# Kernel optimization log

Hardware: AMD Instinct MI355X
Metric: run time of the kernel (lower is better)

Reference implementation:

```python
import jax, jax.numpy as jnp
import numpy as np

B, SQ, SK, D, H, DH = 4, 1024, 1024, 1024, 16, 64  # transform_units*head_units == 1024


def setup_inputs() -> dict:
    key = jax.random.key(0)
    ks = jax.random.split(key, 8)
    q = jax.random.normal(ks[0], (B, SQ, D), dtype=jnp.float32)
    v = jax.random.normal(ks[1], (B, SK, D), dtype=jnp.float32)
    q_mask = jax.random.randint(ks[2], (B, SQ), 0, 2).astype(bool).at[:, 0].set(True)
    v_mask = jax.random.randint(ks[3], (B, SK), 0, 2).astype(bool).at[:, 0].set(True)
    s = 0.02
    Wq = jax.random.normal(ks[4], (D, H * DH), dtype=jnp.float32) * s
    Wk = jax.random.normal(ks[5], (D, H * DH), dtype=jnp.float32) * s
    Wv = jax.random.normal(ks[6], (D, H * DH), dtype=jnp.float32) * s
    Wo = jax.random.normal(ks[7], (H * DH, D), dtype=jnp.float32) * s
    bq = jnp.zeros((H * DH,), jnp.float32)
    bk = jnp.zeros((H * DH,), jnp.float32)
    bv = jnp.zeros((H * DH,), jnp.float32)
    bo = jnp.zeros((D,), jnp.float32)
    return {"q": q, "v": v, "q_mask": q_mask, "v_mask": v_mask,
            "Wq": Wq, "bq": bq, "Wk": Wk, "bk": bk, "Wv": Wv, "bv": bv,
            "Wo": Wo, "bo": bo}


def reference(q, v, q_mask, v_mask, Wq, bq, Wk, bk, Wv, bv, Wo, bo):
    # k = v in the original module
    k = v
    # QKV projections; split-last-dim + batch-concat trick == reshape to heads
    Q = (q @ Wq + bq).reshape(B, SQ, H, DH)
    Kh = (k @ Wk + bk).reshape(B, SK, H, DH)
    V = (v @ Wv + bv).reshape(B, SK, H, DH)
    # Keras Attention: unscaled dot-product scores
    scores = jnp.einsum('bqhd,bkhd->bhqk', Q, Kh)  # [B,H,SQ,SK]
    scores = jnp.where(v_mask[:, None, None, :], scores, jnp.float32(-1e9))
    attn = jax.nn.softmax(scores, axis=-1)
    ctx = jnp.einsum('bhqk,bkhd->bqhd', attn, V).reshape(B, SQ, H * DH)
    # Keras Attention zeros masked query positions before output dense
    ctx = ctx * q_mask[:, :, None].astype(ctx.dtype)
    return ctx @ Wo + bo
```

## Files before the change

kernel.cpp:

```cpp
#include <hip/hip_runtime.h>
#include <hip/hip_fp16.h>

typedef __attribute__((ext_vector_type(8))) _Float16 f16x8;
typedef __attribute__((ext_vector_type(4))) float f32x4;

__global__ __launch_bounds__(256) void cvt_kernel(const float* __restrict__ in,
                                                  _Float16* __restrict__ out, int n4) {
  int i = blockIdx.x * 256 + threadIdx.x;
  if (i < n4) {
    float4 f = ((const float4*)in)[i];
    union { _Float16 h[4]; uint2 u; } o;
    o.h[0] = (_Float16)f.x; o.h[1] = (_Float16)f.y;
    o.h[2] = (_Float16)f.z; o.h[3] = (_Float16)f.w;
    *(uint2*)&out[4 * i] = o.u;
  }
}

__global__ __launch_bounds__(256) void transpose_cvt_kernel(const float* __restrict__ W,
                                                            _Float16* __restrict__ WT) {
  __shared__ float tile[32][33];
  int bx = blockIdx.x * 32, by = blockIdx.y * 32;
  int tx = threadIdx.x & 31, ty = threadIdx.x >> 5;
  for (int i = 0; i < 4; i++)
    tile[ty + 8 * i][tx] = W[(size_t)(by + ty + 8 * i) * 1024 + bx + tx];
  __syncthreads();
  for (int i = 0; i < 4; i++)
    WT[(size_t)(bx + ty + 8 * i) * 1024 + by + tx] = (_Float16)tile[tx][ty + 8 * i];
}

template <typename OutT>
__device__ __forceinline__ void gemm_body(const _Float16* __restrict__ A,
                                          const _Float16* __restrict__ BT,
                                          const float* __restrict__ bias,
                                          OutT* __restrict__ C,
                                          int m0, int n0, int K, int N) {
  __shared__ _Float16 Alds[128 * 72];
  __shared__ _Float16 Blds[128 * 72];
  int tid = threadIdx.x, lane = tid & 63, w = tid >> 6;
  int c = lane & 15, g = lane >> 4;
  int wm = (w & 1) * 64, wn = (w >> 1) * 64;

  f32x4 acc[4][4];
  for (int i = 0; i < 4; i++)
    for (int j = 0; j < 4; j++)
      acc[i][j] = (f32x4){0.f, 0.f, 0.f, 0.f};

  for (int kt = 0; kt < K; kt += 64) {
    __syncthreads();
    for (int p = 0; p < 4; p++) {
      int linear = p * 256 + tid;
      int row = linear >> 3, seg = (linear & 7) * 8;
      *(uint4*)&Alds[row * 72 + seg] = *(const uint4*)&A[(size_t)(m0 + row) * K + kt + seg];
      *(uint4*)&Blds[row * 72 + seg] = *(const uint4*)&BT[(size_t)(n0 + row) * K + kt + seg];
    }
    __syncthreads();
    for (int ks = 0; ks < 2; ks++) {
      f16x8 af[4], bf[4];
      for (int i = 0; i < 4; i++)
        af[i] = *(const f16x8*)&Alds[(wm + i * 16 + c) * 72 + ks * 32 + g * 8];
      for (int j = 0; j < 4; j++)
        bf[j] = *(const f16x8*)&Blds[(wn + j * 16 + c) * 72 + ks * 32 + g * 8];
      for (int i = 0; i < 4; i++)
        for (int j = 0; j < 4; j++)
          acc[i][j] = __builtin_amdgcn_mfma_f32_16x16x32_f16(af[i], bf[j], acc[i][j], 0, 0, 0);
    }
  }
  for (int j = 0; j < 4; j++) {
    float bv = bias[n0 + wn + j * 16 + c];
    for (int i = 0; i < 4; i++) {
      int r = m0 + wm + i * 16 + g * 4;
      int cc = n0 + wn + j * 16 + c;
      for (int e = 0; e < 4; e++)
        C[(size_t)(r + e) * N + cc] = (OutT)(acc[i][j][e] + bv);
    }
  }
}

__global__ __launch_bounds__(256, 3) void gemm_qkv_kernel(
    const _Float16* __restrict__ q16, const _Float16* __restrict__ v16,
    const _Float16* __restrict__ WqT, const _Float16* __restrict__ WkT,
    const _Float16* __restrict__ WvT,
    const float* __restrict__ bq, const float* __restrict__ bk, const float* __restrict__ bv,
    _Float16* __restrict__ Q16, _Float16* __restrict__ K16, _Float16* __restrict__ V16) {
  int z = blockIdx.z;
  const _Float16* A = (z == 0) ? q16 : v16;
  const _Float16* BT = (z == 0) ? WqT : ((z == 1) ? WkT : WvT);
  const float* bias = (z == 0) ? bq : ((z == 1) ? bk : bv);
  _Float16* C = (z == 0) ? Q16 : ((z == 1) ? K16 : V16);
  gemm_body<_Float16>(A, BT, bias, C, blockIdx.y * 128, blockIdx.x * 128, 1024, 1024);
}

__global__ __launch_bounds__(256, 3) void gemm_out_kernel(
    const _Float16* __restrict__ ctx16, const _Float16* __restrict__ WoT,
    const float* __restrict__ bo, float* __restrict__ out) {
  gemm_body<float>(ctx16, WoT, bo, out, blockIdx.y * 128, blockIdx.x * 128, 1024, 1024);
}

__global__ __launch_bounds__(256, 2) void attn_kernel(
    const _Float16* __restrict__ Q16, const _Float16* __restrict__ K16,
    const _Float16* __restrict__ V16,
    const int* __restrict__ q_mask, const int* __restrict__ v_mask,
    _Float16* __restrict__ ctx16) {
  int qb = blockIdx.x, h = blockIdx.y, b = blockIdx.z;
  int tid = threadIdx.x, lane = tid & 63, w = tid >> 6;
  int c = lane & 15, g = lane >> 4;

  __shared__ _Float16 Qlds[128][72];
  __shared__ _Float16 Klds[64][72];
  __shared__ _Float16 VTlds[64][72];
  __shared__ _Float16 Plds[4][32][72];
  __shared__ float maskadd[64];
  __shared__ float qmaskf[128];

  const _Float16* Qbase = Q16 + ((size_t)(b * 1024 + qb * 128)) * 1024 + h * 64;
  for (int p = 0; p < 4; p++) {
    int linear = p * 256 + tid;
    int row = linear >> 3, seg = (linear & 7) * 8;
    *(uint4*)&Qlds[row][seg] = *(const uint4*)&Qbase[(size_t)row * 1024 + seg];
  }
  if (tid < 128) qmaskf[tid] = q_mask[b * 1024 + qb * 128 + tid] ? 1.0f : 0.0f;
  __syncthreads();

  f16x8 qf[2][2];
  for (int i = 0; i < 2; i++)
    for (int ks = 0; ks < 2; ks++)
      qf[i][ks] = *(const f16x8*)&Qlds[w * 32 + i * 16 + c][ks * 32 + g * 8];

  float m_run[2][4], l_run[2][4];
  f32x4 acc_o[2][4];
  for (int i = 0; i < 2; i++)
    for (int e = 0; e < 4; e++) { m_run[i][e] = -3e38f; l_run[i][e] = 0.f; }
  for (int i = 0; i < 2; i++)
    for (int jd = 0; jd < 4; jd++)
      acc_o[i][jd] = (f32x4){0.f, 0.f, 0.f, 0.f};

  const _Float16* Kbase = K16 + ((size_t)(b * 1024)) * 1024 + h * 64;
  const _Float16* Vbase = V16 + ((size_t)(b * 1024)) * 1024 + h * 64;

  for (int kb = 0; kb < 16; kb++) {
    __syncthreads();
    for (int p = 0; p < 2; p++) {
      int linear = p * 256 + tid;
      int row = linear >> 3, seg = (linear & 7) * 8;
      *(uint4*)&Klds[row][seg] = *(const uint4*)&Kbase[(size_t)(kb * 64 + row) * 1024 + seg];
      union { uint4 u; _Float16 hh[8]; } dv;
      dv.u = *(const uint4*)&Vbase[(size_t)(kb * 64 + row) * 1024 + seg];
      for (int e = 0; e < 8; e++) VTlds[seg + e][row] = dv.hh[e];
    }
    if (tid < 64) maskadd[tid] = v_mask[b * 1024 + kb * 64 + tid] ? 0.0f : -1e30f;
    __syncthreads();

    f16x8 kf[4][2];
    for (int j = 0; j < 4; j++)
      for (int ks = 0; ks < 2; ks++)
        kf[j][ks] = *(const f16x8*)&Klds[j * 16 + c][ks * 32 + g * 8];
    f32x4 s[2][4];
    for (int i = 0; i < 2; i++)
      for (int j = 0; j < 4; j++) {
        s[i][j] = (f32x4){0.f, 0.f, 0.f, 0.f};
        s[i][j] = __builtin_amdgcn_mfma_f32_16x16x32_f16(qf[i][0], kf[j][0], s[i][j], 0, 0, 0);
        s[i][j] = __builtin_amdgcn_mfma_f32_16x16x32_f16(qf[i][1], kf[j][1], s[i][j], 0, 0, 0);
      }

    for (int i = 0; i < 2; i++) {
      float mx[4], nm[4], sc[4], rs[4];
      for (int e = 0; e < 4; e++) {
        for (int j = 0; j < 4; j++) s[i][j][e] += maskadd[j * 16 + c];
        mx[e] = fmaxf(fmaxf(s[i][0][e], s[i][1][e]), fmaxf(s[i][2][e], s[i][3][e]));
      }
      for (int e = 0; e < 4; e++) {
        for (int xm = 1; xm < 16; xm <<= 1) mx[e] = fmaxf(mx[e], __shfl_xor(mx[e], xm));
        nm[e] = fmaxf(m_run[i][e], mx[e]);
        sc[e] = __expf(m_run[i][e] - nm[e]);
        m_run[i][e] = nm[e];
      }
      for (int e = 0; e < 4; e++) {
        rs[e] = 0.f;
        for (int j = 0; j < 4; j++) {
          float pv = __expf(s[i][j][e] - nm[e]);
          s[i][j][e] = pv;
          rs[e] += pv;
        }
        for (int xm = 1; xm < 16; xm <<= 1) rs[e] += __shfl_xor(rs[e], xm);
        l_run[i][e] = l_run[i][e] * sc[e] + rs[e];
        for (int jd = 0; jd < 4; jd++) acc_o[i][jd][e] *= sc[e];
      }
      for (int j = 0; j < 4; j++)
        for (int e = 0; e < 4; e++)
          Plds[w][i * 16 + g * 4 + e][j * 16 + c] = (_Float16)s[i][j][e];
    }
    __syncthreads();

    f16x8 pf[2], vf[4];
    for (int ks = 0; ks < 2; ks++) {
      for (int i = 0; i < 2; i++)
        pf[i] = *(const f16x8*)&Plds[w][i * 16 + c][ks * 32 + g * 8];
      for (int jd = 0; jd < 4; jd++)
        vf[jd] = *(const f16x8*)&VTlds[jd * 16 + c][ks * 32 + g * 8];
      for (int i = 0; i < 2; i++)
        for (int jd = 0; jd < 4; jd++)
          acc_o[i][jd] = __builtin_amdgcn_mfma_f32_16x16x32_f16(pf[i], vf[jd], acc_o[i][jd], 0, 0, 0);
    }
  }

  size_t orow_base = ((size_t)(b * 1024 + qb * 128 + w * 32)) * 1024 + h * 64;
  for (int i = 0; i < 2; i++) {
    float rsc[4];
    for (int e = 0; e < 4; e++)
      rsc[e] = qmaskf[w * 32 + i * 16 + g * 4 + e] / l_run[i][e];
    for (int jd = 0; jd < 4; jd++)
      for (int e = 0; e < 4; e++) {
        float val = acc_o[i][jd][e] * rsc[e];
        ctx16[orow_base + (size_t)(i * 16 + g * 4 + e) * 1024 + jd * 16 + c] = (_Float16)val;
      }
  }
}

extern "C" void kernel_launch(void* const* d_in, const int* in_sizes, int n_in,
                              void* d_out, int out_size, void* d_ws, size_t ws_size,
                              hipStream_t stream) {
  const float* q  = (const float*)d_in[0];
  const float* v  = (const float*)d_in[1];
  const int* q_mask = (const int*)d_in[2];
  const int* v_mask = (const int*)d_in[3];
  const float* Wq = (const float*)d_in[4];
  const float* bq = (const float*)d_in[5];
  const float* Wk = (const float*)d_in[6];
  const float* bk = (const float*)d_in[7];
  const float* Wv = (const float*)d_in[8];
  const float* bv = (const float*)d_in[9];
  const float* Wo = (const float*)d_in[10];
  const float* bo = (const float*)d_in[11];
  float* out = (float*)d_out;

  _Float16* ws = (_Float16*)d_ws;
  const size_t NE = (size_t)4 * 1024 * 1024;
  _Float16* q16   = ws;
  _Float16* v16   = ws + NE;
  _Float16* Q16   = ws + 2 * NE;
  _Float16* K16   = ws + 3 * NE;
  _Float16* V16   = ws + 4 * NE;
  _Float16* ctx16 = ws + 5 * NE;
  _Float16* WqT   = ws + 6 * NE;
  _Float16* WkT   = WqT + 1024 * 1024;
  _Float16* WvT   = WkT + 1024 * 1024;
  _Float16* WoT   = WvT + 1024 * 1024;

  cvt_kernel<<<4096, 256, 0, stream>>>(q, q16, (int)(NE / 4));
  cvt_kernel<<<4096, 256, 0, stream>>>(v, v16, (int)(NE / 4));
  dim3 tg(32, 32);
  transpose_cvt_kernel<<<tg, 256, 0, stream>>>(Wq, WqT);
  transpose_cvt_kernel<<<tg, 256, 0, stream>>>(Wk, WkT);
  transpose_cvt_kernel<<<tg, 256, 0, stream>>>(Wv, WvT);
  transpose_cvt_kernel<<<tg, 256, 0, stream>>>(Wo, WoT);
  gemm_qkv_kernel<<<dim3(8, 32, 3), 256, 0, stream>>>(q16, v16, WqT, WkT, WvT,
                                                      bq, bk, bv, Q16, K16, V16);
  attn_kernel<<<dim3(8, 16, 4), 256, 0, stream>>>(Q16, K16, V16, q_mask, v_mask, ctx16);
  gemm_out_kernel<<<dim3(8, 32), 256, 0, stream>>>(ctx16, WoT, bo, out);
}
```

Before: 247.1 us.

## Use direct global-to-LDS loads, pre-transpose V, double-buffer attention, fuse prep launches

```diff
diff --git a/kernel.cpp b/kernel.cpp
--- a/kernel.cpp
+++ b/kernel.cpp
@@ -4,20 +4,33 @@
 typedef __attribute__((ext_vector_type(8))) _Float16 f16x8;
 typedef __attribute__((ext_vector_type(4))) float f32x4;
 
-__global__ __launch_bounds__(256) void cvt_kernel(const float* __restrict__ in,
-                                                  _Float16* __restrict__ out, int n4) {
+__device__ __forceinline__ void gload_lds16(const _Float16* g, _Float16* l) {
+  __builtin_amdgcn_global_load_lds((const __attribute__((address_space(1))) void*)g,
+                                   (__attribute__((address_space(3))) void*)l, 16, 0, 0);
+}
+
+__global__ __launch_bounds__(256) void cvt2_kernel(const float* __restrict__ q,
+                                                   const float* __restrict__ v,
+                                                   _Float16* __restrict__ q16,
+                                                   _Float16* __restrict__ v16) {
   int i = blockIdx.x * 256 + threadIdx.x;
-  if (i < n4) {
-    float4 f = ((const float4*)in)[i];
-    union { _Float16 h[4]; uint2 u; } o;
-    o.h[0] = (_Float16)f.x; o.h[1] = (_Float16)f.y;
-    o.h[2] = (_Float16)f.z; o.h[3] = (_Float16)f.w;
-    *(uint2*)&out[4 * i] = o.u;
-  }
-}
-
-__global__ __launch_bounds__(256) void transpose_cvt_kernel(const float* __restrict__ W,
-                                                            _Float16* __restrict__ WT) {
+  const float* in = blockIdx.y ? v : q;
+  _Float16* out = blockIdx.y ? v16 : q16;
+  float4 f = ((const float4*)in)[i];
+  union { _Float16 h[4]; uint2 u; } o;
+  o.h[0] = (_Float16)f.x; o.h[1] = (_Float16)f.y;
+  o.h[2] = (_Float16)f.z; o.h[3] = (_Float16)f.w;
+  *(uint2*)&out[4 * i] = o.u;
+}
+
+__global__ __launch_bounds__(256) void transpose_cvt4_kernel(
+    const float* __restrict__ W0, const float* __restrict__ W1,
+    const float* __restrict__ W2, const float* __restrict__ W3,
+    _Float16* __restrict__ T0, _Float16* __restrict__ T1,
+    _Float16* __restrict__ T2, _Float16* __restrict__ T3) {
+  int z = blockIdx.z;
+  const float* W = (z == 0) ? W0 : (z == 1) ? W1 : (z == 2) ? W2 : W3;
+  _Float16* T = (z == 0) ? T0 : (z == 1) ? T1 : (z == 2) ? T2 : T3;
   __shared__ float tile[32][33];
   int bx = blockIdx.x * 32, by = blockIdx.y * 32;
   int tx = threadIdx.x & 31, ty = threadIdx.x >> 5;
@@ -25,7 +38,28 @@
     tile[ty + 8 * i][tx] = W[(size_t)(by + ty + 8 * i) * 1024 + bx + tx];
   __syncthreads();
   for (int i = 0; i < 4; i++)
-    WT[(size_t)(bx + ty + 8 * i) * 1024 + by + tx] = (_Float16)tile[tx][ty + 8 * i];
+    T[(size_t)(bx + ty + 8 * i) * 1024 + by + tx] = (_Float16)tile[tx][ty + 8 * i];
+}
+
+__global__ __launch_bounds__(256) void transpose_v_kernel(const _Float16* __restrict__ V16,
+                                                          _Float16* __restrict__ VT16) {
+  __shared__ _Float16 tile[64][72];
+  int kb = blockIdx.x, h = blockIdx.y, b = blockIdx.z;
+  int tid = threadIdx.x;
+  for (int p = 0; p < 2; p++) {
+    int lin = p * 256 + tid;
+    int row = lin >> 3, seg = (lin & 7) * 8;
+    *(uint4*)&tile[row][seg] =
+        *(const uint4*)&V16[(size_t)(b * 1024 + kb * 64 + row) * 1024 + h * 64 + seg];
+  }
+  __syncthreads();
+  for (int p = 0; p < 2; p++) {
+    int lin = p * 256 + tid;
+    int dh = lin >> 3, seg = (lin & 7) * 8;
+    union { uint4 u; _Float16 hh[8]; } o;
+    for (int e = 0; e < 8; e++) o.hh[e] = tile[seg + e][dh];
+    *(uint4*)&VT16[((size_t)((b * 16 + h) * 64 + dh)) * 1024 + kb * 64 + seg] = o.u;
+  }
 }
 
 template <typename OutT>
@@ -34,11 +68,23 @@
                                           const float* __restrict__ bias,
                                           OutT* __restrict__ C,
                                           int m0, int n0, int K, int N) {
-  __shared__ _Float16 Alds[128 * 72];
-  __shared__ _Float16 Blds[128 * 72];
+  __shared__ _Float16 Alds[128 * 64];
+  __shared__ _Float16 Blds[128 * 64];
   int tid = threadIdx.x, lane = tid & 63, w = tid >> 6;
   int c = lane & 15, g = lane >> 4;
   int wm = (w & 1) * 64, wn = (w >> 1) * 64;
+  int lr = lane >> 3, ls = (lane & 7) * 8;
+
+  const _Float16* ga[4]; const _Float16* gb[4];
+  _Float16* la[4]; _Float16* lb[4];
+  for (int p = 0; p < 4; p++) {
+    int chunk = w * 4 + p;
+    int row = chunk * 8 + lr;
+    ga[p] = &A[(size_t)(m0 + row) * K + ls];
+    gb[p] = &BT[(size_t)(n0 + row) * K + ls];
+    la[p] = Alds + chunk * 512;
+    lb[p] = Blds + chunk * 512;
+  }
 
   f32x4 acc[4][4];
   for (int i = 0; i < 4; i++)
@@ -48,18 +94,16 @@
   for (int kt = 0; kt < K; kt += 64) {
     __syncthreads();
     for (int p = 0; p < 4; p++) {
-      int linear = p * 256 + tid;
-      int row = linear >> 3, seg = (linear & 7) * 8;
-      *(uint4*)&Alds[row * 72 + seg] = *(const uint4*)&A[(size_t)(m0 + row) * K + kt + seg];
-      *(uint4*)&Blds[row * 72 + seg] = *(const uint4*)&BT[(size_t)(n0 + row) * K + kt + seg];
+      gload_lds16(ga[p] + kt, la[p]);
+      gload_lds16(gb[p] + kt, lb[p]);
     }
     __syncthreads();
     for (int ks = 0; ks < 2; ks++) {
       f16x8 af[4], bf[4];
       for (int i = 0; i < 4; i++)
-        af[i] = *(const f16x8*)&Alds[(wm + i * 16 + c) * 72 + ks * 32 + g * 8];
+        af[i] = *(const f16x8*)&Alds[(wm + i * 16 + c) * 64 + ks * 32 + g * 8];
       for (int j = 0; j < 4; j++)
-        bf[j] = *(const f16x8*)&Blds[(wn + j * 16 + c) * 72 + ks * 32 + g * 8];
+        bf[j] = *(const f16x8*)&Blds[(wn + j * 16 + c) * 64 + ks * 32 + g * 8];
       for (int i = 0; i < 4; i++)
         for (int j = 0; j < 4; j++)
           acc[i][j] = __builtin_amdgcn_mfma_f32_16x16x32_f16(af[i], bf[j], acc[i][j], 0, 0, 0);
@@ -76,7 +120,7 @@
   }
 }
 
-__global__ __launch_bounds__(256, 3) void gemm_qkv_kernel(
+__global__ __launch_bounds__(256) void gemm_qkv_kernel(
     const _Float16* __restrict__ q16, const _Float16* __restrict__ v16,
     const _Float16* __restrict__ WqT, const _Float16* __restrict__ WkT,
     const _Float16* __restrict__ WvT,
@@ -90,130 +134,147 @@
   gemm_body<_Float16>(A, BT, bias, C, blockIdx.y * 128, blockIdx.x * 128, 1024, 1024);
 }
 
-__global__ __launch_bounds__(256, 3) void gemm_out_kernel(
+__global__ __launch_bounds__(256) void gemm_out_kernel(
     const _Float16* __restrict__ ctx16, const _Float16* __restrict__ WoT,
     const float* __restrict__ bo, float* __restrict__ out) {
   gemm_body<float>(ctx16, WoT, bo, out, blockIdx.y * 128, blockIdx.x * 128, 1024, 1024);
 }
 
-__global__ __launch_bounds__(256, 2) void attn_kernel(
+__global__ __launch_bounds__(256, 4) void attn_kernel(
     const _Float16* __restrict__ Q16, const _Float16* __restrict__ K16,
-    const _Float16* __restrict__ V16,
+    const _Float16* __restrict__ VT16,
     const int* __restrict__ q_mask, const int* __restrict__ v_mask,
     _Float16* __restrict__ ctx16) {
   int qb = blockIdx.x, h = blockIdx.y, b = blockIdx.z;
   int tid = threadIdx.x, lane = tid & 63, w = tid >> 6;
   int c = lane & 15, g = lane >> 4;
-
-  __shared__ _Float16 Qlds[128][72];
-  __shared__ _Float16 Klds[64][72];
-  __shared__ _Float16 VTlds[64][72];
-  __shared__ _Float16 Plds[4][32][72];
-  __shared__ float maskadd[64];
-  __shared__ float qmaskf[128];
-
-  const _Float16* Qbase = Q16 + ((size_t)(b * 1024 + qb * 128)) * 1024 + h * 64;
-  for (int p = 0; p < 4; p++) {
-    int linear = p * 256 + tid;
-    int row = linear >> 3, seg = (linear & 7) * 8;
-    *(uint4*)&Qlds[row][seg] = *(const uint4*)&Qbase[(size_t)row * 1024 + seg];
-  }
-  if (tid < 128) qmaskf[tid] = q_mask[b * 1024 + qb * 128 + tid] ? 1.0f : 0.0f;
+  int lr = lane >> 3, ls = lane & 7;
+
+  __shared__ _Float16 QP[64 * 64];
+  __shared__ _Float16 Kl[2][64 * 64];
+  __shared__ _Float16 Vl[2][64 * 64];
+
+  const _Float16* Qg = Q16 + ((size_t)(b * 1024 + qb * 64)) * 1024 + h * 64;
+  const _Float16* Kg = K16 + ((size_t)(b * 1024)) * 1024 + h * 64;
+  const _Float16* Vg = VT16 + ((size_t)(b * 16 + h)) * 64 * 1024;
+
+  int row0 = w * 16 + lr, row1 = row0 + 8;
+  int kx = (ls ^ lr) * 8;
+  int ch0 = w * 2, ch1 = w * 2 + 1;
+
+  gload_lds16(Qg + (size_t)row0 * 1024 + kx, QP + ch0 * 512);
+  gload_lds16(Qg + (size_t)row1 * 1024 + kx, QP + ch1 * 512);
+  gload_lds16(Kg + (size_t)row0 * 1024 + kx, &Kl[0][ch0 * 512]);
+  gload_lds16(Kg + (size_t)row1 * 1024 + kx, &Kl[0][ch1 * 512]);
+  gload_lds16(Vg + (size_t)row0 * 1024 + kx, &Vl[0][ch0 * 512]);
+  gload_lds16(Vg + (size_t)row1 * 1024 + kx, &Vl[0][ch1 * 512]);
   __syncthreads();
 
-  f16x8 qf[2][2];
-  for (int i = 0; i < 2; i++)
-    for (int ks = 0; ks < 2; ks++)
-      qf[i][ks] = *(const f16x8*)&Qlds[w * 32 + i * 16 + c][ks * 32 + g * 8];
-
-  float m_run[2][4], l_run[2][4];
-  f32x4 acc_o[2][4];
-  for (int i = 0; i < 2; i++)
-    for (int e = 0; e < 4; e++) { m_run[i][e] = -3e38f; l_run[i][e] = 0.f; }
-  for (int i = 0; i < 2; i++)
-    for (int jd = 0; jd < 4; jd++)
-      acc_o[i][jd] = (f32x4){0.f, 0.f, 0.f, 0.f};
-
-  const _Float16* Kbase = K16 + ((size_t)(b * 1024)) * 1024 + h * 64;
-  const _Float16* Vbase = V16 + ((size_t)(b * 1024)) * 1024 + h * 64;
-
+  f16x8 qf[2];
+  {
+    int row = w * 16 + c;
+    const char* rb = (const char*)QP + row * 128;
+    int x = (row & 7) << 4;
+    qf[0] = *(const f16x8*)(rb + ((g * 16) ^ x));
+    qf[1] = *(const f16x8*)(rb + ((64 + g * 16) ^ x));
+  }
+
+  float m_run[4], l_run[4];
+  f32x4 acc_o[4];
+  for (int e = 0; e < 4; e++) { m_run[e] = -3e38f; l_run[e] = 0.f; }
+  for (int jd = 0; jd < 4; jd++) acc_o[jd] = (f32x4){0.f, 0.f, 0.f, 0.f};
+
+  char* pb = (char*)QP;
+  int cur = 0;
   for (int kb = 0; kb < 16; kb++) {
+    if (kb + 1 < 16) {
+      int nb = cur ^ 1;
+      const _Float16* kgs = Kg + (size_t)(kb + 1) * 64 * 1024;
+      const _Float16* vgs = Vg + (kb + 1) * 64;
+      gload_lds16(kgs + (size_t)row0 * 1024 + kx, &Kl[nb][ch0 * 512]);
+      gload_lds16(kgs + (size_t)row1 * 1024 + kx, &Kl[nb][ch1 * 512]);
+      gload_lds16(vgs + (size_t)row0 * 1024 + kx, &Vl[nb][ch0 * 512]);
+      gload_lds16(vgs + (size_t)row1 * 1024 + kx, &Vl[nb][ch1 * 512]);
+    }
+    float madd[4];
+    for (int j = 0; j < 4; j++)
+      madd[j] = v_mask[b * 1024 + kb * 64 + j * 16 + c] ? 0.f : -1e30f;
+
+    f32x4 s[4];
+    const char* kbse = (const char*)&Kl[cur][0];
+    for (int j = 0; j < 4; j++) {
+      int row = j * 16 + c;
+      const char* rb = kbse + row * 128;
+      int x = (row & 7) << 4;
+      f16x8 k0 = *(const f16x8*)(rb + ((g * 16) ^ x));
+      f16x8 k1 = *(const f16x8*)(rb + ((64 + g * 16) ^ x));
+      s[j] = (f32x4){0.f, 0.f, 0.f, 0.f};
+      s[j] = __builtin_amdgcn_mfma_f32_16x16x32_f16(qf[0], k0, s[j], 0, 0, 0);
+      s[j] = __builtin_amdgcn_mfma_f32_16x16x32_f16(qf[1], k1, s[j], 0, 0, 0);
+    }
+
+    for (int e = 0; e < 4; e++) {
+      float v0 = s[0][e] + madd[0], v1 = s[1][e] + madd[1];
+      float v2 = s[2][e] + madd[2], v3 = s[3][e] + madd[3];
+      s[0][e] = v0; s[1][e] = v1; s[2][e] = v2; s[3][e] = v3;
+      float mx = fmaxf(fmaxf(v0, v1), fmaxf(v2, v3));
+      mx = fmaxf(mx, __shfl_xor(mx, 1));
+      mx = fmaxf(mx, __shfl_xor(mx, 2));
+      mx = fmaxf(mx, __shfl_xor(mx, 4));
+      mx = fmaxf(mx, __shfl_xor(mx, 8));
+      float nm = fmaxf(m_run[e], mx);
+      float sc = __expf(m_run[e] - nm);
+      m_run[e] = nm;
+      float rs = 0.f;
+      for (int j = 0; j < 4; j++) {
+        float pv = __expf(s[j][e] - nm);
+        s[j][e] = pv;
+        rs += pv;
+      }
+      rs += __shfl_xor(rs, 1);
+      rs += __shfl_xor(rs, 2);
+      rs += __shfl_xor(rs, 4);
+      rs += __shfl_xor(rs, 8);
+      l_run[e] = l_run[e] * sc + rs;
+      for (int jd = 0; jd < 4; jd++) acc_o[jd][e] *= sc;
+    }
+
+    for (int j = 0; j < 4; j++)
+      for (int e = 0; e < 4; e++) {
+        int prow = w * 16 + g * 4 + e;
+        int pby = prow * 128 + (((j * 16 + c) * 2) ^ ((prow & 7) << 4));
+        *(_Float16*)(pb + pby) = (_Float16)s[j][e];
+      }
+    asm volatile("s_waitcnt lgkmcnt(0)" ::: "memory");
+    __builtin_amdgcn_sched_barrier(0);
+
+    const char* vbse = (const char*)&Vl[cur][0];
+    for (int ks = 0; ks < 2; ks++) {
+      int prow = w * 16 + c;
+      f16x8 pf = *(const f16x8*)(pb + prow * 128 +
+                                 ((ks * 64 + g * 16) ^ ((prow & 7) << 4)));
+      for (int jd = 0; jd < 4; jd++) {
+        int vrow = jd * 16 + c;
+        f16x8 vf = *(const f16x8*)(vbse + vrow * 128 +
+                                   ((ks * 64 + g * 16) ^ ((vrow & 7) << 4)));
+        acc_o[jd] = __builtin_amdgcn_mfma_f32_16x16x32_f16(pf, vf, acc_o[jd], 0, 0, 0);
+      }
+    }
+
     __syncthreads();
-    for (int p = 0; p < 2; p++) {
-      int linear = p * 256 + tid;
-      int row = linear >> 3, seg = (linear & 7) * 8;
-      *(uint4*)&Klds[row][seg] = *(const uint4*)&Kbase[(size_t)(kb * 64 + row) * 1024 + seg];
-      union { uint4 u; _Float16 hh[8]; } dv;
-      dv.u = *(const uint4*)&Vbase[(size_t)(kb * 64 + row) * 1024 + seg];
-      for (int e = 0; e < 8; e++) VTlds[seg + e][row] = dv.hh[e];
-    }
-    if (tid < 64) maskadd[tid] = v_mask[b * 1024 + kb * 64 + tid] ? 0.0f : -1e30f;
-    __syncthreads();
-
-    f16x8 kf[4][2];
-    for (int j = 0; j < 4; j++)
-      for (int ks = 0; ks < 2; ks++)
-        kf[j][ks] = *(const f16x8*)&Klds[j * 16 + c][ks * 32 + g * 8];
-    f32x4 s[2][4];
-    for (int i = 0; i < 2; i++)
-      for (int j = 0; j < 4; j++) {
-        s[i][j] = (f32x4){0.f, 0.f, 0.f, 0.f};
-        s[i][j] = __builtin_amdgcn_mfma_f32_16x16x32_f16(qf[i][0], kf[j][0], s[i][j], 0, 0, 0);
-        s[i][j] = __builtin_amdgcn_mfma_f32_16x16x32_f16(qf[i][1], kf[j][1], s[i][j], 0, 0, 0);
-      }
-
-    for (int i = 0; i < 2; i++) {
-      float mx[4], nm[4], sc[4], rs[4];
-      for (int e = 0; e < 4; e++) {
-        for (int j = 0; j < 4; j++) s[i][j][e] += maskadd[j * 16 + c];
-        mx[e] = fmaxf(fmaxf(s[i][0][e], s[i][1][e]), fmaxf(s[i][2][e], s[i][3][e]));
-      }
-      for (int e = 0; e < 4; e++) {
-        for (int xm = 1; xm < 16; xm <<= 1) mx[e] = fmaxf(mx[e], __shfl_xor(mx[e], xm));
-        nm[e] = fmaxf(m_run[i][e], mx[e]);
-        sc[e] = __expf(m_run[i][e] - nm[e]);
-        m_run[i][e] = nm[e];
-      }
-      for (int e = 0; e < 4; e++) {
-        rs[e] = 0.f;
-        for (int j = 0; j < 4; j++) {
-          float pv = __expf(s[i][j][e] - nm[e]);
-          s[i][j][e] = pv;
-          rs[e] += pv;
-        }
-        for (int xm = 1; xm < 16; xm <<= 1) rs[e] += __shfl_xor(rs[e], xm);
-        l_run[i][e] = l_run[i][e] * sc[e] + rs[e];
-        for (int jd = 0; jd < 4; jd++) acc_o[i][jd][e] *= sc[e];
-      }
-      for (int j = 0; j < 4; j++)
-        for (int e = 0; e < 4; e++)
-          Plds[w][i * 16 + g * 4 + e][j * 16 + c] = (_Float16)s[i][j][e];
-    }
-    __syncthreads();
-
-    f16x8 pf[2], vf[4];
-    for (int ks = 0; ks < 2; ks++) {
-      for (int i = 0; i < 2; i++)
-        pf[i] = *(const f16x8*)&Plds[w][i * 16 + c][ks * 32 + g * 8];
-      for (int jd = 0; jd < 4; jd++)
-        vf[jd] = *(const f16x8*)&VTlds[jd * 16 + c][ks * 32 + g * 8];
-      for (int i = 0; i < 2; i++)
-        for (int jd = 0; jd < 4; jd++)
-          acc_o[i][jd] = __builtin_amdgcn_mfma_f32_16x16x32_f16(pf[i], vf[jd], acc_o[i][jd], 0, 0, 0);
-    }
-  }
-
-  size_t orow_base = ((size_t)(b * 1024 + qb * 128 + w * 32)) * 1024 + h * 64;
-  for (int i = 0; i < 2; i++) {
-    float rsc[4];
+    cur ^= 1;
+  }
+
+  int qrow = b * 1024 + qb * 64 + w * 16 + g * 4;
+  float inv[4];
+  for (int e = 0; e < 4; e++) {
+    float qm = q_mask[qrow + e] ? 1.0f : 0.0f;
+    inv[e] = qm / l_run[e];
+  }
+  _Float16* cb = ctx16 + ((size_t)qrow) * 1024 + h * 64;
+  for (int jd = 0; jd < 4; jd++)
     for (int e = 0; e < 4; e++)
-      rsc[e] = qmaskf[w * 32 + i * 16 + g * 4 + e] / l_run[i][e];
-    for (int jd = 0; jd < 4; jd++)
-      for (int e = 0; e < 4; e++) {
-        float val = acc_o[i][jd][e] * rsc[e];
-        ctx16[orow_base + (size_t)(i * 16 + g * 4 + e) * 1024 + jd * 16 + c] = (_Float16)val;
-      }
-  }
+      cb[(size_t)e * 1024 + jd * 16 + c] = (_Float16)(acc_o[jd][e] * inv[e]);
 }
 
 extern "C" void kernel_launch(void* const* d_in, const int* in_sizes, int n_in,
@@ -245,16 +306,13 @@
   _Float16* WkT   = WqT + 1024 * 1024;
   _Float16* WvT   = WkT + 1024 * 1024;
   _Float16* WoT   = WvT + 1024 * 1024;
-
-  cvt_kernel<<<4096, 256, 0, stream>>>(q, q16, (int)(NE / 4));
-  cvt_kernel<<<4096, 256, 0, stream>>>(v, v16, (int)(NE / 4));
-  dim3 tg(32, 32);
-  transpose_cvt_kernel<<<tg, 256, 0, stream>>>(Wq, WqT);
-  transpose_cvt_kernel<<<tg, 256, 0, stream>>>(Wk, WkT);
-  transpose_cvt_kernel<<<tg, 256, 0, stream>>>(Wv, WvT);
-  transpose_cvt_kernel<<<tg, 256, 0, stream>>>(Wo, WoT);
+  _Float16* VT16  = q16;
+
+  cvt2_kernel<<<dim3(4096, 2), 256, 0, stream>>>(q, v, q16, v16);
+  transpose_cvt4_kernel<<<dim3(32, 32, 4), 256, 0, stream>>>(Wq, Wk, Wv, Wo, WqT, WkT, WvT, WoT);
   gemm_qkv_kernel<<<dim3(8, 32, 3), 256, 0, stream>>>(q16, v16, WqT, WkT, WvT,
                                                       bq, bk, bv, Q16, K16, V16);
-  attn_kernel<<<dim3(8, 16, 4), 256, 0, stream>>>(Q16, K16, V16, q_mask, v_mask, ctx16);
+  transpose_v_kernel<<<dim3(16, 16, 4), 256, 0, stream>>>(V16, VT16);
+  attn_kernel<<<dim3(16, 16, 4), 256, 0, stream>>>(Q16, K16, VT16, q_mask, v_mask, ctx16);
   gemm_out_kernel<<<dim3(8, 32), 256, 0, stream>>>(ctx16, WoT, bo, out);
 }
```

Measured after the change: 245.2 us. Within noise of the previous version (-0.8%).
